# Performance work log

Hardware: AMD Instinct MI355X
Metric: run time of the kernel (lower is better)

## Reference

```python
import jax, jax.numpy as jnp
import numpy as np

H, K, TP = 15, 15, 8          # h bits, k=c*h candidates per bit, tp coordinates
NLOC = 2 ** H                  # 32768 code space
NNODES, BATCH, DMAX = 100000, 128, 64
EPS, GAMMA, ALPHA, POS_RATIO = 0.1, 2.0, 1.0, 1.0
NCAND = H * K + 1              # 226 connection candidates


def setup_inputs() -> dict:
    key = jax.random.key(0)
    k1, k2, k3, k4, k5, k6, k7 = jax.random.split(key, 7)
    degree = jax.random.randint(k1, (NNODES,), 1, DMAX + 1, dtype=jnp.int32)
    locations = jax.random.randint(k2, (NNODES, TP), 0, NLOC, dtype=jnp.int32)
    sta_ind = jax.random.permutation(k3, NNODES)[:BATCH].astype(jnp.int32)  # unique batch nodes
    lg = degree[sta_ind]
    mask = jnp.arange(DMAX, dtype=jnp.int32)[None, :] < lg[:, None]         # [B,D] valid neighbors
    pos_ind = jnp.where(mask, jax.random.randint(k4, (BATCH, DMAX), 0, NNODES, dtype=jnp.int32), -1)
    neg_ind = jnp.where(mask, jax.random.randint(k5, (BATCH, DMAX), 0, NNODES, dtype=jnp.int32), -1)
    upper = (jnp.int32(1) << jnp.arange(H, dtype=jnp.int32))                # 2^j per flipped bit
    random_masks = jax.random.randint(k6, (BATCH, H, K, TP), 0, NLOC, dtype=jnp.int32) % upper[None, :, None, None]
    perm = jax.random.permutation(k7, NCAND).astype(jnp.int32)              # candidate shuffle
    xs = jnp.arange(NLOC)
    lut = jnp.where(xs == 0, 0.0,
                    jnp.floor(jnp.log2(jnp.maximum(xs, 1).astype(jnp.float32))) + 1.0).astype(jnp.float32)
    return {"lut": lut, "sta_ind": sta_ind, "locations": locations, "degree": degree,
            "pos_ind": pos_ind, "neg_ind": neg_ind, "random_masks": random_masks, "perm": perm}


def _p(lut_dis, degree, sta_ind, ig2):
    # p(dis, ig1, ig2) from the torch module; ig2 may contain -1 (torch wraps to last row)
    deg1 = degree[sta_ind][:, None]                                   # [B,1]
    ig2w = jnp.where(ig2 < 0, ig2 + NNODES, ig2)
    deg2 = degree[ig2w]                                               # [B,D]
    log_ap = jnp.log(((deg1 + 1) * (deg2 + 1)).astype(jnp.float32))   # [B,D]
    aa = (lut_dis + EPS) / log_ap[:, :, None, None]
    return 1.0 / (1.0 + aa ** GAMMA / ALPHA)


def reference(lut, sta_ind, locations, degree, pos_ind, neg_ind, random_masks, perm):
    mask = pos_ind != -1                                              # [B,D]
    lg = mask.sum(axis=1).astype(jnp.float32)                         # == degree[sta_ind]
    sta_loc = locations[sta_ind]                                      # [B,tp]
    pos_loc = jnp.where(mask[:, :, None], locations[jnp.where(mask, pos_ind, 0)], -1)  # [B,D,tp]
    neg_loc = jnp.where(mask[:, :, None], locations[jnp.where(mask, neg_ind, 0)], -1)

    # connection(): flip each of H bits, XOR with K random low-bit masks, plus the original point
    flip = (jnp.int32(1) << jnp.arange(H, dtype=jnp.int32))[None, :, None]
    flipped = sta_loc[:, None, :] ^ flip                              # [B,H,tp]
    cand = (flipped[:, :, None, :] ^ random_masks).reshape(sta_loc.shape[0], H * K, TP)
    cnc_loc = jnp.concatenate([cand, sta_loc[:, None, :]], axis=1)[:, perm, :]  # [B,C,tp]

    m1 = mask[:, :, None]                                             # [B,D,1]
    m2 = mask[:, :, None, None]                                       # [B,D,1,1]

    def dist(xor, m):
        return jnp.where(m, lut[jnp.where(m, xor, 0)], -1.0)

    dis_sta_pos = dist(sta_loc[:, None, :] ^ pos_loc, m1)             # [B,D,tp]
    dis_sta_posum = dis_sta_pos.sum(axis=-1)                          # [B,D]
    dis_sta_neg = dist(sta_loc[:, None, :] ^ neg_loc, m1)
    dis_sta_negum = dis_sta_neg.sum(axis=-1)

    dis_pos_cnc = dist(cnc_loc[:, None, :, :] ^ pos_loc[:, :, None, :], m2)  # [B,D,C,tp]
    dis_neg_cnc = dist(cnc_loc[:, None, :, :] ^ neg_loc[:, :, None, :], m2)

    dis_new_pos = jnp.where(m2, (dis_pos_cnc - dis_sta_pos[:, :, None, :]
                                 + dis_sta_posum[:, :, None, None]) / TP, 0.0)
    dis_new_neg = jnp.where(m2, (dis_neg_cnc - dis_sta_neg[:, :, None, :]
                                 + dis_sta_negum[:, :, None, None]) / TP, 1000.0)

    pos_loss = -jnp.sum(jnp.log(_p(dis_new_pos, degree, sta_ind, pos_ind)), axis=1) / lg[:, None, None]
    neg_loss = -jnp.sum(jnp.log(1.0 + EPS - _p(dis_new_neg, degree, sta_ind, neg_ind)), axis=1) / lg[:, None, None]
    total_loss = POS_RATIO * pos_loss + neg_loss                      # [B,C,tp]

    index = jnp.argmin(total_loss, axis=1)                            # [B,tp] best candidate per coord
    sel_loc = jnp.take_along_axis(cnc_loc, index[:, None, :], axis=1)[:, 0, :]  # [B,tp]
    new_locations = locations.at[sta_ind].set(sel_loc)                # scatter update

    def gather_sel(x):
        return jnp.take_along_axis(x, index[:, None, :], axis=1)[:, 0, :]

    tl = jnp.mean(gather_sel(total_loss))
    pl = jnp.mean(gather_sel(pos_loss))
    nl = jnp.mean(gather_sel(neg_loss))
    return (jnp.stack([tl, pl, nl]), new_locations)
```

## Files before the change

### kernel.cpp

```cpp
#include <hip/hip_runtime.h>
#include <math.h>

constexpr int TPC    = 8;
constexpr int NNODES = 100000;
constexpr int BATCH  = 128;
constexpr int DMAX   = 64;
constexpr int Hc     = 15;
constexpr int Kc     = 15;
constexpr int NCAND  = Hc * Kc + 1;
constexpr int NLOCF  = NNODES * TPC;


__launch_bounds__(256)
__global__ void main_kernel(const float* __restrict__ lut,
                            const int* __restrict__ sta_ind,
                            const int* __restrict__ locations,
                            const int* __restrict__ degree,
                            const int* __restrict__ pos_ind,
                            const int* __restrict__ neg_ind,
                            const int* __restrict__ rmasks,
                            const int* __restrict__ perm,
                            float* __restrict__ wsf,
                            int*   __restrict__ wsi,
                            float* __restrict__ out) {
    __shared__ float Tp[64][32];
    __shared__ float Tn[64][32];
    __shared__ int   ploc[64], nloc[64];
    __shared__ int   Sarr[2][64];
    __shared__ float Lsq[2][64];
    __shared__ float logLsq[64];
    __shared__ int   dsarr[2][64];
    __shared__ int   varr[2][64];
    __shared__ int   sh_sta[8];
    __shared__ int   powlut[16];
    __shared__ float lg_sh;
    __shared__ float cpos[256], cneg[256];
    __shared__ int   cval_sh[256];
    __shared__ float wmin[4];
    __shared__ int   widx[4];

    const int bid = blockIdx.x;
    const int b   = bid >> 3;
    const int t   = bid & 7;
    const int tid = threadIdx.x;
    const int sta = sta_ind[b];

    for (int idx = bid * 256 + tid; idx < NLOCF; idx += 1024 * 256)
        out[3 + idx] = (float)locations[idx];

    if (tid < 8) sh_sta[tid] = locations[sta * 8 + tid];
    if (tid >= 16 && tid < 32) {
        const int i = tid - 16;
        powlut[i] = (i == 0) ? (int)lut[0] : (int)lut[1 << (i - 1)];
    }
    __syncthreads();

    if (tid < 128) {
        const int which = tid >> 6;
        const int d     = tid & 63;
        const int* ind  = which ? neg_ind : pos_ind;
        const int pi    = ind[b * DMAX + d];
        const int valid = (pi >= 0) ? 1 : 0;
        const int piw   = valid ? pi : pi + NNODES;
        const int deg1  = degree[sta];
        const int deg2  = degree[piw];
        const float L   = logf((float)((deg1 + 1) * (deg2 + 1)));
        int Si = 0, dsi = 0, lc = 0;
        if (valid) {
            const int4* lp = reinterpret_cast<const int4*>(locations + pi * 8);
            const int4 va = lp[0], vb = lp[1];
            const int l0[8] = {va.x, va.y, va.z, va.w, vb.x, vb.y, vb.z, vb.w};
            #pragma unroll
            for (int tt = 0; tt < 8; ++tt) {
                const int x   = sh_sta[tt] ^ l0[tt];
                const int idx = 32 - __clz(x);
                const int bl  = ((x & (x - 1)) == 0) ? powlut[idx] : idx;
                Si += bl;
                if (tt == t) { dsi = bl; lc = l0[tt]; }
            }
        }
        const float lsq = L * L;
        Sarr[which][d]  = Si;
        Lsq[which][d]   = lsq;
        if (which == 0) logLsq[d] = logf(lsq);
        dsarr[which][d] = dsi;
        varr[which][d]  = valid;
        if (which == 0) ploc[d] = lc; else nloc[d] = lc;
        if (which == 0) {
            unsigned long long m = __ballot(valid);
            if (tid == 0) lg_sh = (float)__popcll(m);
        }
    }
    __syncthreads();

    for (int e = tid; e < 4096; e += 256) {
        const int which = e >> 11;
        const int rem   = e & 2047;
        const int d     = rem >> 5;
        const int slot  = rem & 31;
        const int g     = (slot < 16) ? slot : powlut[slot - 16];
        const float lsq = Lsq[which][d];
        float x;
        if (varr[which][d])
            x = (float)(g - dsarr[which][d] + Sarr[which][d]) * 0.125f;
        else
            x = which ? 1000.0f : 0.0f;
        const float y  = x + 0.1f;
        const float s  = lsq + y * y;
        const float ls = logf(s);
        float term;
        if (which) term = ls - logf(0.1f * lsq + 1.1f * y * y);
        else       term = ls - logLsq[d];
        if (which) Tn[d][slot] = term; else Tp[d][slot] = term;
    }
    __syncthreads();

    const int c = tid;
    float v = __builtin_inff();
    float plc = 0.0f, nlc = 0.0f;
    int cval = 0;
    if (c < NCAND) {
        const int q  = perm[c];
        const int st = sh_sta[t];
        if (q < NCAND - 1) {
            const int h = q / Kc, k = q % Kc;
            cval = st ^ (1 << h) ^ rmasks[((b * Hc + h) * Kc + k) * 8 + t];
        } else {
            cval = st;
        }
        float ps = 0.0f, ns = 0.0f;
        #pragma unroll 8
        for (int d = 0; d < 64; ++d) {
            const int xp = cval ^ ploc[d];
            const int bp = 32 - __clz(xp);
            ps += Tp[d][((xp & (xp - 1)) == 0) ? bp + 16 : bp];
            const int xn = cval ^ nloc[d];
            const int bn = 32 - __clz(xn);
            ns += Tn[d][((xn & (xn - 1)) == 0) ? bn + 16 : bn];
        }
        const float lg = lg_sh;
        plc = ps / lg;
        nlc = ns / lg;
        v   = plc + nlc;
    }
    cpos[tid]    = plc;
    cneg[tid]    = nlc;
    cval_sh[tid] = cval;

    int idx = tid;
    #pragma unroll
    for (int m = 32; m >= 1; m >>= 1) {
        const float ov = __shfl_xor(v, m, 64);
        const int   oi = __shfl_xor(idx, m, 64);
        if (ov < v || (ov == v && oi < idx)) { v = ov; idx = oi; }
    }
    if ((tid & 63) == 0) { wmin[tid >> 6] = v; widx[tid >> 6] = idx; }
    __syncthreads();

    if (tid == 0) {
        float bv = wmin[0];
        int   bi = widx[0];
        #pragma unroll
        for (int w = 1; w < 4; ++w) {
            const float vv = wmin[w];
            const int   ii = widx[w];
            if (vv < bv || (vv == bv && ii < bi)) { bv = vv; bi = ii; }
        }
        wsf[bid]        = bv;
        wsf[1024 + bid] = cpos[bi];
        wsf[2048 + bid] = cneg[bi];
        wsi[bid]        = cval_sh[bi];
    }
}

__launch_bounds__(256)
__global__ void finish_kernel(const int* __restrict__ sta_ind,
                              const float* __restrict__ wsf,
                              const int* __restrict__ wsi,
                              float* __restrict__ out) {
    const int tid = threadIdx.x;
    __shared__ float wsum[3][4];
    #pragma unroll
    for (int a = 0; a < 3; ++a) {
        float s = 0.0f;
        #pragma unroll
        for (int j = 0; j < 4; ++j) s += wsf[a * 1024 + j * 256 + tid];
        #pragma unroll
        for (int m = 32; m >= 1; m >>= 1) s += __shfl_xor(s, m, 64);
        if ((tid & 63) == 0) wsum[a][tid >> 6] = s;
    }
    #pragma unroll
    for (int j = 0; j < 4; ++j) {
        const int i = j * 256 + tid;
        const int b = i >> 3, t = i & 7;
        out[3 + sta_ind[b] * 8 + t] = (float)wsi[i];
    }
    __syncthreads();
    if (tid < 3)
        out[tid] = (wsum[tid][0] + wsum[tid][1] + wsum[tid][2] + wsum[tid][3])
                   * (1.0f / 1024.0f);
}

extern "C" void kernel_launch(void* const* d_in, const int* in_sizes, int n_in,
                              void* d_out, int out_size, void* d_ws, size_t ws_size,
                              hipStream_t stream) {
    const float* lut     = (const float*)d_in[0];
    const int* sta_ind   = (const int*)d_in[1];
    const int* locations = (const int*)d_in[2];
    const int* degree    = (const int*)d_in[3];
    const int* pos_ind   = (const int*)d_in[4];
    const int* neg_ind   = (const int*)d_in[5];
    const int* rmasks    = (const int*)d_in[6];
    const int* perm      = (const int*)d_in[7];
    float* out = (float*)d_out;
    float* wsf = (float*)d_ws;
    int*   wsi = (int*)d_ws + 3072;

    hipLaunchKernelGGL(main_kernel, dim3(BATCH * TPC), dim3(256), 0, stream,
                       lut, sta_ind, locations, degree, pos_ind, neg_ind, rmasks, perm,
                       wsf, wsi, out);
    hipLaunchKernelGGL(finish_kernel, dim3(1), dim3(256), 0, stream,
                       sta_ind, wsf, wsi, out);
}
```

Baseline: 95.67 us.

## Split pos/neg sums across 512 threads and fuse finish via last-block atomics

Doubles the block to 512 threads so the positive and negative 64-neighbor sums for each candidate run in separate halves, then combines them through shared memory. The separate finish kernel is removed. Its reduction and scatter now run in whichever block is last to finish, detected with a two-level atomic counter reset by a memset. This trades one kernel launch for a memset plus atomics and fences, and the larger block may lower occupancy per CU.

```diff
diff --git a/kernel.cpp b/kernel.cpp
--- a/kernel.cpp
+++ b/kernel.cpp
@@ -11,7 +11,7 @@
 constexpr int NLOCF  = NNODES * TPC;
 
 
-__launch_bounds__(256)
+__launch_bounds__(512)
 __global__ void main_kernel(const float* __restrict__ lut,
                             const int* __restrict__ sta_ind,
                             const int* __restrict__ locations,
@@ -22,6 +22,7 @@
                             const int* __restrict__ perm,
                             float* __restrict__ wsf,
                             int*   __restrict__ wsi,
+                            unsigned* __restrict__ counters,
                             float* __restrict__ out) {
     __shared__ float Tp[64][32];
     __shared__ float Tn[64][32];
@@ -34,10 +35,12 @@
     __shared__ int   sh_sta[8];
     __shared__ int   powlut[16];
     __shared__ float lg_sh;
-    __shared__ float cpos[256], cneg[256];
+    __shared__ float part[512];
     __shared__ int   cval_sh[256];
     __shared__ float wmin[4];
     __shared__ int   widx[4];
+    __shared__ int   lastflag;
+    __shared__ float wsum[3][4];
 
     const int bid = blockIdx.x;
     const int b   = bid >> 3;
@@ -45,7 +48,9 @@
     const int tid = threadIdx.x;
     const int sta = sta_ind[b];
 
-    for (int idx = bid * 256 + tid; idx < NLOCF; idx += 1024 * 256)
+    if (tid == 0) lastflag = 0;
+
+    for (int idx = bid * 512 + tid; idx < NLOCF; idx += 1024 * 512)
         out[3 + idx] = (float)locations[idx];
 
     if (tid < 8) sh_sta[tid] = locations[sta * 8 + tid];
@@ -93,7 +98,7 @@
     }
     __syncthreads();
 
-    for (int e = tid; e < 4096; e += 256) {
+    for (int e = tid; e < 4096; e += 512) {
         const int which = e >> 11;
         const int rem   = e & 2047;
         const int d     = rem >> 5;
@@ -115,9 +120,9 @@
     }
     __syncthreads();
 
-    const int c = tid;
-    float v = __builtin_inff();
-    float plc = 0.0f, nlc = 0.0f;
+    const int half = tid >> 8;
+    const int c    = tid & 255;
+    float acc = 0.0f;
     int cval = 0;
     if (c < NCAND) {
         const int q  = perm[c];
@@ -128,33 +133,39 @@
         } else {
             cval = st;
         }
-        float ps = 0.0f, ns = 0.0f;
-        #pragma unroll 8
-        for (int d = 0; d < 64; ++d) {
-            const int xp = cval ^ ploc[d];
-            const int bp = 32 - __clz(xp);
-            ps += Tp[d][((xp & (xp - 1)) == 0) ? bp + 16 : bp];
-            const int xn = cval ^ nloc[d];
-            const int bn = 32 - __clz(xn);
-            ns += Tn[d][((xn & (xn - 1)) == 0) ? bn + 16 : bn];
-        }
+        if (half == 0) {
+            #pragma unroll 8
+            for (int d = 0; d < 64; ++d) {
+                const int xp = cval ^ ploc[d];
+                const int bp = 32 - __clz(xp);
+                acc += Tp[d][((xp & (xp - 1)) == 0) ? bp + 16 : bp];
+            }
+            cval_sh[c] = cval;
+        } else {
+            #pragma unroll 8
+            for (int d = 0; d < 64; ++d) {
+                const int xn = cval ^ nloc[d];
+                const int bn = 32 - __clz(xn);
+                acc += Tn[d][((xn & (xn - 1)) == 0) ? bn + 16 : bn];
+            }
+        }
+    }
+    part[tid] = acc;
+    __syncthreads();
+
+    float v = __builtin_inff();
+    if (tid < 256 && c < NCAND) {
         const float lg = lg_sh;
-        plc = ps / lg;
-        nlc = ns / lg;
-        v   = plc + nlc;
-    }
-    cpos[tid]    = plc;
-    cneg[tid]    = nlc;
-    cval_sh[tid] = cval;
-
-    int idx = tid;
+        v = part[tid] / lg + part[tid + 256] / lg;
+    }
+    int idx = tid & 255;
     #pragma unroll
     for (int m = 32; m >= 1; m >>= 1) {
         const float ov = __shfl_xor(v, m, 64);
         const int   oi = __shfl_xor(idx, m, 64);
         if (ov < v || (ov == v && oi < idx)) { v = ov; idx = oi; }
     }
-    if ((tid & 63) == 0) { wmin[tid >> 6] = v; widx[tid >> 6] = idx; }
+    if (tid < 256 && (tid & 63) == 0) { wmin[tid >> 6] = v; widx[tid >> 6] = idx; }
     __syncthreads();
 
     if (tid == 0) {
@@ -166,39 +177,44 @@
             const int   ii = widx[w];
             if (vv < bv || (vv == bv && ii < bi)) { bv = vv; bi = ii; }
         }
+        const float lg = lg_sh;
         wsf[bid]        = bv;
-        wsf[1024 + bid] = cpos[bi];
-        wsf[2048 + bid] = cneg[bi];
+        wsf[1024 + bid] = part[bi] / lg;
+        wsf[2048 + bid] = part[256 + bi] / lg;
         wsi[bid]        = cval_sh[bi];
-    }
-}
-
-__launch_bounds__(256)
-__global__ void finish_kernel(const int* __restrict__ sta_ind,
-                              const float* __restrict__ wsf,
-                              const int* __restrict__ wsi,
-                              float* __restrict__ out) {
-    const int tid = threadIdx.x;
-    __shared__ float wsum[3][4];
-    #pragma unroll
-    for (int a = 0; a < 3; ++a) {
-        float s = 0.0f;
-        #pragma unroll
-        for (int j = 0; j < 4; ++j) s += wsf[a * 1024 + j * 256 + tid];
-        #pragma unroll
-        for (int m = 32; m >= 1; m >>= 1) s += __shfl_xor(s, m, 64);
-        if ((tid & 63) == 0) wsum[a][tid >> 6] = s;
-    }
-    #pragma unroll
-    for (int j = 0; j < 4; ++j) {
-        const int i = j * 256 + tid;
-        const int b = i >> 3, t = i & 7;
-        out[3 + sta_ind[b] * 8 + t] = (float)wsi[i];
-    }
-    __syncthreads();
-    if (tid < 3)
-        out[tid] = (wsum[tid][0] + wsum[tid][1] + wsum[tid][2] + wsum[tid][3])
-                   * (1.0f / 1024.0f);
+        __threadfence();
+        const unsigned g1 = atomicAdd(&counters[bid & 31], 1u);
+        if (g1 == 31) {
+            const unsigned g2 = atomicAdd(&counters[32], 1u);
+            if (g2 == 31) lastflag = 1;
+        }
+    }
+    __syncthreads();
+
+    if (lastflag) {
+        __threadfence();
+        if (tid < 256) {
+            #pragma unroll
+            for (int a = 0; a < 3; ++a) {
+                float s = 0.0f;
+                #pragma unroll
+                for (int j = 0; j < 4; ++j) s += wsf[a * 1024 + j * 256 + tid];
+                #pragma unroll
+                for (int m = 32; m >= 1; m >>= 1) s += __shfl_xor(s, m, 64);
+                if ((tid & 63) == 0) wsum[a][tid >> 6] = s;
+            }
+            #pragma unroll
+            for (int j = 0; j < 4; ++j) {
+                const int i  = j * 256 + tid;
+                const int bb = i >> 3, tt = i & 7;
+                out[3 + sta_ind[bb] * 8 + tt] = (float)wsi[i];
+            }
+        }
+        __syncthreads();
+        if (tid < 3)
+            out[tid] = (wsum[tid][0] + wsum[tid][1] + wsum[tid][2] + wsum[tid][3])
+                       * (1.0f / 1024.0f);
+    }
 }
 
 extern "C" void kernel_launch(void* const* d_in, const int* in_sizes, int n_in,
@@ -213,12 +229,12 @@
     const int* rmasks    = (const int*)d_in[6];
     const int* perm      = (const int*)d_in[7];
     float* out = (float*)d_out;
-    float* wsf = (float*)d_ws;
-    int*   wsi = (int*)d_ws + 3072;
-
-    hipLaunchKernelGGL(main_kernel, dim3(BATCH * TPC), dim3(256), 0, stream,
+    float*    wsf      = (float*)d_ws;
+    int*      wsi      = (int*)((char*)d_ws + 12288);
+    unsigned* counters = (unsigned*)((char*)d_ws + 16384);
+
+    hipMemsetAsync(counters, 0, 33 * sizeof(unsigned), stream);
+    hipLaunchKernelGGL(main_kernel, dim3(BATCH * TPC), dim3(512), 0, stream,
                        lut, sta_ind, locations, degree, pos_ind, neg_ind, rmasks, perm,
-                       wsf, wsi, out);
-    hipLaunchKernelGGL(finish_kernel, dim3(1), dim3(256), 0, stream,
-                       sta_ind, wsf, wsi, out);
+                       wsf, wsi, counters, out);
 }
```

Result: slower. 113.1 us (+18.2%).
